# Kernel tuning notes

Hardware: AMD Instinct MI355X
Metric: run time of the kernel (lower is better)

The kernel has to match this reference:

```python
import jax, jax.numpy as jnp
import numpy as np

B, L, LTXT = 4, 1024, 128
D_MODEL, TEXT_DIM = 768, 768
D_INNER, D_STATE, D_CONV, DT_RANK = 2 * D_MODEL, 16, 4, (D_MODEL + 15) // 16


def setup_inputs() -> dict:
    key = jax.random.key(0)
    ks = jax.random.split(key, 10)
    s = 0.02
    f32 = jnp.float32
    # A_log init as in mamba_ssm: A = repeat(arange(1, d_state+1))
    A_log = jnp.log(jnp.broadcast_to(jnp.arange(1, D_STATE + 1, dtype=f32), (D_INNER, D_STATE)))
    return {
        "image_tokens": jax.random.normal(ks[0], (B, L, D_MODEL), f32),
        "text_tokens": jax.random.normal(ks[1], (B, LTXT, TEXT_DIM), f32),
        "W_txt": s * jax.random.normal(ks[2], (D_MODEL, TEXT_DIM), f32),
        "b_txt": jnp.zeros((D_MODEL,), f32),
        "in_proj_w": s * jax.random.normal(ks[3], (2 * D_INNER, D_MODEL), f32),
        "conv_w": s * jax.random.normal(ks[4], (D_INNER, 1, D_CONV), f32),
        "conv_b": jnp.zeros((D_INNER,), f32),
        "x_proj_w": s * jax.random.normal(ks[5], (DT_RANK + 2 * D_STATE, D_INNER), f32),
        "dt_proj_w": s * jax.random.normal(ks[6], (D_INNER, DT_RANK), f32),
        "dt_proj_b": jnp.full((D_INNER,), -4.6, f32),  # inv-softplus of small dt init
        "A_log": A_log,
        "D": jnp.ones((D_INNER,), f32),
        "out_proj_w": s * jax.random.normal(ks[7], (D_MODEL, D_INNER), f32),
    }


def _mamba(tokens, in_proj_w, conv_w, conv_b, x_proj_w, dt_proj_w, dt_proj_b, A_log, D, out_proj_w):
    Bsz = tokens.shape[0]
    # input projection -> x, z each (B, L, d_inner)
    xz = tokens @ in_proj_w.T
    x, z = jnp.split(xz, 2, axis=-1)
    # causal depthwise conv1d over L + SiLU
    x_bdl = jnp.transpose(x, (0, 2, 1))  # (B, d_inner, L)
    x_conv = jax.lax.conv_general_dilated(
        x_bdl, conv_w, (1,), [(D_CONV - 1, 0)],
        dimension_numbers=("NCH", "OIH", "NCH"), feature_group_count=D_INNER,
    ) + conv_b[None, :, None]
    x = jax.nn.silu(jnp.transpose(x_conv, (0, 2, 1)))  # (B, L, d_inner)
    # input-dependent SSM params
    x_dbl = x @ x_proj_w.T  # (B, L, dt_rank + 2*d_state)
    dt_r = x_dbl[..., :DT_RANK]
    Bm = x_dbl[..., DT_RANK:DT_RANK + D_STATE]  # (B, L, d_state)
    Cm = x_dbl[..., DT_RANK + D_STATE:]         # (B, L, d_state)
    dt = jax.nn.softplus(dt_r @ dt_proj_w.T + dt_proj_b)  # (B, L, d_inner)
    A = -jnp.exp(A_log)  # (d_inner, d_state)

    def step(h, inp):
        dt_t, B_t, C_t, u_t = inp  # (B,d_inner),(B,d_state),(B,d_state),(B,d_inner)
        dA = jnp.exp(dt_t[:, :, None] * A)                  # (B, d_inner, d_state)
        h = dA * h + (dt_t * u_t)[:, :, None] * B_t[:, None, :]
        y = jnp.einsum("bds,bs->bd", h, C_t)
        return h, y

    h0 = jnp.zeros((Bsz, D_INNER, D_STATE), tokens.dtype)
    xs = (
        jnp.transpose(dt, (1, 0, 2)),
        jnp.transpose(Bm, (1, 0, 2)),
        jnp.transpose(Cm, (1, 0, 2)),
        jnp.transpose(x, (1, 0, 2)),
    )
    _, ys = jax.lax.scan(step, h0, xs)  # ys: (L, B, d_inner)
    y = jnp.transpose(ys, (1, 0, 2)) + x * D
    y = y * jax.nn.silu(z)
    return y @ out_proj_w.T  # (B, L, d_model)


def reference(image_tokens, text_tokens, W_txt, b_txt, in_proj_w, conv_w, conv_b,
              x_proj_w, dt_proj_w, dt_proj_b, A_log, D, out_proj_w):
    # text_pool='cls' -> take token 0
    txt = text_tokens[:, 0, :] @ W_txt.T + b_txt          # (B, d_model)
    tokens = image_tokens + txt[:, None, :]                # broadcast add
    y = _mamba(tokens, in_proj_w, conv_w, conv_b, x_proj_w,
               dt_proj_w, dt_proj_b, A_log, D, out_proj_w)
    # AdaptiveAvgPool1d(1) over sequence dim, then squeeze -> (B, d_model)
    return y.mean(axis=1)
```

## Files before the change

kernel.cpp:

```cpp
#include <hip/hip_runtime.h>
#include <math.h>

constexpr int kB   = 4;
constexpr int kL   = 1024;
constexpr int kDM  = 768;
constexpr int kDI  = 1536;
constexpr int kDS  = 16;
constexpr int kDTR = 48;
constexpr int kNX  = 80;
constexpr int kM   = kB * kL;
constexpr int kLTXT = 128;

typedef __attribute__((ext_vector_type(8))) short bf16x8;
typedef __attribute__((ext_vector_type(4))) float f32x4;

__device__ inline unsigned short f2bf(float f) {
    unsigned u = __float_as_uint(f);
    u = (u + 0x7FFFu + ((u >> 16) & 1u)) >> 16;
    return (unsigned short)u;
}

__device__ __forceinline__ void gl2lds16(const unsigned short* g, unsigned short* l) {
    __builtin_amdgcn_global_load_lds(
        (const __attribute__((address_space(1))) unsigned int*)g,
        (__attribute__((address_space(3))) unsigned int*)l, 16, 0, 0);
}

__global__ __launch_bounds__(256) void txt_kernel(
    const float* __restrict__ text, const float* __restrict__ Wt,
    const float* __restrict__ bt, float* __restrict__ txt)
{
    int gw = blockIdx.x * 4 + (threadIdx.x >> 6);
    int lane = threadIdx.x & 63;
    int b = gw / kDM;
    int j = gw - b * kDM;
    const float* trow = text + (size_t)b * kLTXT * kDM;
    const float* wrow = Wt + (size_t)j * kDM;
    float acc = 0.f;
    for (int k = lane; k < kDM; k += 64) acc = fmaf(trow[k], wrow[k], acc);
    #pragma unroll
    for (int o = 32; o; o >>= 1) acc += __shfl_xor(acc, o, 64);
    if (lane == 0) txt[gw] = acc + bt[j];
}

__global__ __launch_bounds__(256) void tokens_bf16_kernel(
    const float* __restrict__ img, const float* __restrict__ txt,
    unsigned short* __restrict__ tok)
{
    int i = blockIdx.x * 256 + threadIdx.x;
    float4 a = ((const float4*)img)[i];
    int m = i / (kDM / 4);
    int k4 = i - m * (kDM / 4);
    float4 tv = ((const float4*)(txt + (size_t)(m >> 10) * kDM))[k4];
    ushort4 o;
    o.x = f2bf(a.x + tv.x); o.y = f2bf(a.y + tv.y);
    o.z = f2bf(a.z + tv.z); o.w = f2bf(a.w + tv.w);
    ((ushort4*)tok)[i] = o;
}

__global__ __launch_bounds__(256) void castw_kernel(
    const float* __restrict__ w, unsigned short* __restrict__ o, int n4)
{
    int i = blockIdx.x * 256 + threadIdx.x;
    if (i >= n4) return;
    float4 a = ((const float4*)w)[i];
    ushort4 v;
    v.x = f2bf(a.x); v.y = f2bf(a.y); v.z = f2bf(a.z); v.w = f2bf(a.w);
    ((ushort4*)o)[i] = v;
}

__global__ __launch_bounds__(256) void mfma_inproj_kernel(
    const unsigned short* __restrict__ A, const unsigned short* __restrict__ W,
    float* __restrict__ xout, float* __restrict__ gout)
{
    __shared__ unsigned short Asm[2][128][32];
    __shared__ unsigned short Wsm[2][128][32];
    const int t = threadIdx.x;
    const int lane = t & 63;
    const int wv = t >> 6;
    const int wr = wv >> 1, wc = wv & 1;
    const int m0 = blockIdx.x * 128;
    const int n0 = blockIdx.y * 128;

    const int srow = lane >> 2;
    const int scol = (lane & 3) * 8;
    const unsigned short* agp  = A + (size_t)(m0 + wv * 32 + srow) * kDM + scol;
    const unsigned short* agp2 = agp + 16 * kDM;
    const unsigned short* wgp  = W + (size_t)(n0 + wv * 32 + srow) * kDM + scol;
    const unsigned short* wgp2 = wgp + 16 * kDM;

    auto stage = [&](int buf, int k0) {
        gl2lds16(agp  + k0, &Asm[buf][wv * 32][0]);
        gl2lds16(agp2 + k0, &Asm[buf][wv * 32 + 16][0]);
        gl2lds16(wgp  + k0, &Wsm[buf][wv * 32][0]);
        gl2lds16(wgp2 + k0, &Wsm[buf][wv * 32 + 16][0]);
    };

    f32x4 acc[4][4] = {};
    const int fr = lane & 15;
    const int fk = (lane >> 4) * 8;

    stage(0, 0);
    __syncthreads();

    int buf = 0;
    for (int k0 = 0; k0 < kDM; k0 += 32) {
        if (k0 + 32 < kDM) stage(buf ^ 1, k0 + 32);
        bf16x8 af[4], wf[4];
        #pragma unroll
        for (int i = 0; i < 4; ++i)
            af[i] = *(const bf16x8*)&Asm[buf][wr * 64 + i * 16 + fr][fk];
        #pragma unroll
        for (int j = 0; j < 4; ++j)
            wf[j] = *(const bf16x8*)&Wsm[buf][wc * 64 + j * 16 + fr][fk];
        #pragma unroll
        for (int i = 0; i < 4; ++i)
            #pragma unroll
            for (int j = 0; j < 4; ++j)
                acc[i][j] = __builtin_amdgcn_mfma_f32_16x16x32_bf16(af[i], wf[j], acc[i][j], 0, 0, 0);
        __syncthreads();
        buf ^= 1;
    }

    const int erow = (lane >> 4) * 4;
    const int ecol = lane & 15;
    #pragma unroll
    for (int i = 0; i < 4; ++i) {
        #pragma unroll
        for (int j = 0; j < 4; ++j) {
            const int gn = n0 + wc * 64 + j * 16 + ecol;
            #pragma unroll
            for (int q = 0; q < 4; ++q) {
                const int gm = m0 + wr * 64 + i * 16 + erow + q;
                float v = acc[i][j][q];
                if (gn < kDI) {
                    xout[(size_t)gm * kDI + gn] = v;
                } else {
                    gout[(size_t)gm * kDI + (gn - kDI)] = v / (1.f + __expf(-v));
                }
            }
        }
    }
}

constexpr int kKS   = 8;
constexpr int kKSEG = kDI / kKS;

__global__ __launch_bounds__(256) void xproj_splitk_kernel(
    const float* __restrict__ A, const float* __restrict__ W,
    float* __restrict__ part)
{
    __shared__ float As[16][68];
    __shared__ float Ws[16][84];
    const int t = threadIdx.x;
    const int m0 = blockIdx.x * 64;
    const int kbase = blockIdx.y * kKSEG;
    const int lrow = t >> 2, lk4 = (t & 3) << 2;
    const int ci = (t & 15) << 2;
    const int cj = (t >> 4) * 5;
    float acc[4][5] = {};
    const float* aptr = A + (size_t)(m0 + lrow) * kDI + kbase + lk4;

    for (int k0 = 0; k0 < kKSEG; k0 += 16) {
        float4 av = *(const float4*)(aptr + k0);
        if (k0) __syncthreads();
        As[lk4+0][lrow] = av.x; As[lk4+1][lrow] = av.y;
        As[lk4+2][lrow] = av.z; As[lk4+3][lrow] = av.w;
        #pragma unroll
        for (int i = 0; i < 5; ++i) {
            int idx = t + 256 * i;
            int n = idx % 80;
            int k = idx / 80;
            Ws[k][n] = W[(size_t)n * kDI + kbase + k0 + k];
        }
        __syncthreads();
        #pragma unroll
        for (int k = 0; k < 16; ++k) {
            const float4 a4 = *(const float4*)&As[k][ci];
            const float aa[4] = {a4.x, a4.y, a4.z, a4.w};
            float ww[5];
            #pragma unroll
            for (int j = 0; j < 5; ++j) ww[j] = Ws[k][cj + j];
            #pragma unroll
            for (int i = 0; i < 4; ++i)
                #pragma unroll
                for (int j = 0; j < 5; ++j)
                    acc[i][j] = fmaf(aa[i], ww[j], acc[i][j]);
        }
    }

    float* pbase = part + ((size_t)blockIdx.y * kM) * kNX;
    #pragma unroll
    for (int i = 0; i < 4; ++i)
        #pragma unroll
        for (int j = 0; j < 5; ++j)
            pbase[(size_t)(m0 + ci + i) * kNX + cj + j] = acc[i][j];
}

__global__ __launch_bounds__(256) void xproj_reduce_kernel(
    const float* __restrict__ part, float* __restrict__ xdbl)
{
    int i = blockIdx.x * 256 + threadIdx.x;
    float s = 0.f;
    #pragma unroll
    for (int k = 0; k < kKS; ++k) s += part[(size_t)k * kM * kNX + i];
    xdbl[i] = s;
}

__global__ __launch_bounds__(256) void conv_silu_kernel(
    const float* __restrict__ xraw, const float* __restrict__ cw,
    const float* __restrict__ cb, float* __restrict__ xout)
{
    int i = blockIdx.x * 256 + threadIdx.x;
    int d4 = i % (kDI / 4);
    int ml = i / (kDI / 4);
    int l = ml & (kL - 1);
    const int d = d4 * 4;
    float4 acc = *(const float4*)&cb[d];
    const float* base = xraw + (size_t)ml * kDI + d - 3 * (size_t)kDI;
    float4 w0 = *(const float4*)&cw[(d + 0) * 4];
    float4 w1 = *(const float4*)&cw[(d + 1) * 4];
    float4 w2 = *(const float4*)&cw[(d + 2) * 4];
    float4 w3 = *(const float4*)&cw[(d + 3) * 4];
    const float wj[4][4] = {{w0.x, w1.x, w2.x, w3.x}, {w0.y, w1.y, w2.y, w3.y},
                            {w0.z, w1.z, w2.z, w3.z}, {w0.w, w1.w, w2.w, w3.w}};
    #pragma unroll
    for (int j = 0; j < 4; ++j) {
        if (l - 3 + j >= 0) {
            float4 xv = *(const float4*)(base + (size_t)j * kDI);
            acc.x = fmaf(xv.x, wj[j][0], acc.x);
            acc.y = fmaf(xv.y, wj[j][1], acc.y);
            acc.z = fmaf(xv.z, wj[j][2], acc.z);
            acc.w = fmaf(xv.w, wj[j][3], acc.w);
        }
    }
    acc.x /= (1.f + __expf(-acc.x));
    acc.y /= (1.f + __expf(-acc.y));
    acc.z /= (1.f + __expf(-acc.z));
    acc.w /= (1.f + __expf(-acc.w));
    *(float4*)&xout[(size_t)ml * kDI + d] = acc;
}

constexpr int kT  = 64;
constexpr int kNC = kL / kT;
constexpr int kXP = 84;

__global__ __launch_bounds__(256) void scan3_kernel(
    const float* __restrict__ x, const float* __restrict__ g,
    const float* __restrict__ xdbl, const float* __restrict__ Wd,
    const float* __restrict__ dt_bias,
    const float* __restrict__ A_log, const float* __restrict__ Dvec,
    float* __restrict__ ysum)
{
    __shared__ float xdS[2][kT][kXP];
    __shared__ float uS [2][kT][16];
    __shared__ float gS [2][kT][16];
    __shared__ float dtS[2][kT][17];
    const int t = threadIdx.x;
    const int b  = blockIdx.x / 96;
    const int d0 = (blockIdx.x % 96) * 16;

    const int sl = t >> 2, sc = (t & 3) << 2;
    const float* x_base  = x  + ((size_t)b << 10) * kDI + d0;
    const float* g_base  = g  + ((size_t)b << 10) * kDI + d0;
    const float* xd_base = xdbl + ((size_t)b << 10) * kNX;

    const int s = t & 15;
    const int c = t >> 4;
    const int d = d0 + c;
    const float Aval = -__expf(A_log[d * kDS + s]);

    const int cc = t & 15, ii = t >> 4;
    float4 wreg[12];
    {
        const float* wrow = Wd + (size_t)(d0 + cc) * kDTR;
        #pragma unroll
        for (int i = 0; i < 12; ++i) wreg[i] = *(const float4*)(wrow + i * 4);
    }
    const float bn = dt_bias[d0 + cc];

    float4 r_u, r_g, r_xd[5];
    auto load_chunk = [&](int l0) {
        r_u = *(const float4*)(x_base + (size_t)(l0 + sl) * kDI + sc);
        r_g = *(const float4*)(g_base + (size_t)(l0 + sl) * kDI + sc);
        #pragma unroll
        for (int j = 0; j < 5; ++j) {
            int idx = t + 256 * j;
            int row = idx / 20, col4 = idx % 20;
            r_xd[j] = *(const float4*)(xd_base + (size_t)(l0 + row) * kNX + col4 * 4);
        }
    };
    auto store_chunk = [&](int bf) {
        *(float4*)&uS[bf][sl][sc] = r_u;
        *(float4*)&gS[bf][sl][sc] = r_g;
        #pragma unroll
        for (int j = 0; j < 5; ++j) {
            int idx = t + 256 * j;
            int row = idx / 20, col4 = idx % 20;
            *(float4*)&xdS[bf][row][col4 * 4] = r_xd[j];
        }
    };
    auto compute_dt = [&](int bf) {
        #pragma unroll
        for (int q = 0; q < 4; ++q) {
            const int i = ii * 4 + q;
            float a = bn;
            #pragma unroll
            for (int k4 = 0; k4 < 12; ++k4) {
                const float4 xv = *(const float4*)&xdS[bf][i][k4 * 4];
                a = fmaf(xv.x, wreg[k4].x, a);
                a = fmaf(xv.y, wreg[k4].y, a);
                a = fmaf(xv.z, wreg[k4].z, a);
                a = fmaf(xv.w, wreg[k4].w, a);
            }
            a = (a > 20.f) ? a : log1pf(__expf(a));
            dtS[bf][i][cc] = a;
        }
    };

    load_chunk(0);
    store_chunk(0);
    __syncthreads();
    compute_dt(0);
    __syncthreads();

    float h = 0.f, acc = 0.f, ug = 0.f;
    for (int ck = 0; ck < kNC; ++ck) {
        const int bu = ck & 1;
        if (ck + 1 < kNC) load_chunk((ck + 1) * kT);
        #pragma unroll 4
        for (int i = 0; i < kT; ++i) {
            const float dtv = dtS[bu][i][c];
            const float uv  = uS [bu][i][c];
            const float gv  = gS [bu][i][c];
            const float Bv  = xdS[bu][i][kDTR + s];
            const float Cv  = xdS[bu][i][kDTR + 16 + s];
            const float dA  = __expf(dtv * Aval);
            h   = fmaf(dA, h, dtv * uv * Bv);
            acc = fmaf(h * Cv, gv, acc);
            ug  = fmaf(uv, gv, ug);
        }
        if (ck + 1 < kNC) {
            store_chunk(bu ^ 1);
            __syncthreads();
            compute_dt(bu ^ 1);
            __syncthreads();
        }
    }

    #pragma unroll
    for (int o = 1; o < 16; o <<= 1) acc += __shfl_xor(acc, o, 64);
    if (s == 0) ysum[(size_t)b * kDI + d] = acc + Dvec[d] * ug;
}

__global__ __launch_bounds__(256) void final_kernel(
    const float* __restrict__ ysum, const float* __restrict__ Wout,
    float* __restrict__ out)
{
    int gw = blockIdx.x * 4 + (threadIdx.x >> 6);
    int lane = threadIdx.x & 63;
    int b = gw / kDM;
    int j = gw - b * kDM;
    const float* yrow = ysum + (size_t)b * kDI;
    const float* wrow = Wout + (size_t)j * kDI;
    float acc = 0.f;
    for (int k = lane; k < kDI; k += 64) acc = fmaf(yrow[k], wrow[k], acc);
    #pragma unroll
    for (int o = 32; o; o >>= 1) acc += __shfl_xor(acc, o, 64);
    if (lane == 0) out[gw] = acc * (1.f / (float)kL);
}

extern "C" void kernel_launch(void* const* d_in, const int* in_sizes, int n_in,
                              void* d_out, int out_size, void* d_ws, size_t ws_size,
                              hipStream_t stream)
{
    const float* image_tokens = (const float*)d_in[0];
    const float* text_tokens  = (const float*)d_in[1];
    const float* W_txt        = (const float*)d_in[2];
    const float* b_txt        = (const float*)d_in[3];
    const float* in_proj_w    = (const float*)d_in[4];
    const float* conv_w       = (const float*)d_in[5];
    const float* conv_b       = (const float*)d_in[6];
    const float* x_proj_w     = (const float*)d_in[7];
    const float* dt_proj_w    = (const float*)d_in[8];
    const float* dt_proj_b    = (const float*)d_in[9];
    const float* A_log        = (const float*)d_in[10];
    const float* Dvec         = (const float*)d_in[11];
    const float* out_proj_w   = (const float*)d_in[12];
    float* out = (float*)d_out;

    char* p = (char*)d_ws;
    float* txt = (float*)p;                       p += 12288;
    unsigned short* tokb = (unsigned short*)p;    p += (size_t)kM * kDM * 2;
    unsigned short* wb   = (unsigned short*)p;    p += (size_t)2 * kDI * kDM * 2;
    float* xraw = (float*)p;                      p += (size_t)kM * kDI * 4;
    float* gbuf = (float*)p;                      p += (size_t)kM * kDI * 4;
    float* xbuf = (float*)p;                      p += (size_t)kM * kDI * 4;
    float* xdbl = (float*)p;                      p += (size_t)kM * kNX * 4;
    float* ysum = (float*)p;                      p += (size_t)kB * kDI * 4;
    float* part = (float*)tokb;

    txt_kernel<<<dim3(kB * kDM / 4), dim3(256), 0, stream>>>(text_tokens, W_txt, b_txt, txt);

    tokens_bf16_kernel<<<dim3(kM * kDM / 4 / 256), dim3(256), 0, stream>>>(image_tokens, txt, tokb);

    castw_kernel<<<dim3((2 * kDI * kDM / 4 + 255) / 256), dim3(256), 0, stream>>>(
        in_proj_w, wb, 2 * kDI * kDM / 4);

    mfma_inproj_kernel<<<dim3(kM / 128, 2 * kDI / 128), dim3(256), 0, stream>>>(
        tokb, wb, xraw, gbuf);

    conv_silu_kernel<<<dim3(kM * kDI / 4 / 256), dim3(256), 0, stream>>>(
        xraw, conv_w, conv_b, xbuf);

    xproj_splitk_kernel<<<dim3(kM / 64, kKS), dim3(256), 0, stream>>>(xbuf, x_proj_w, part);
    xproj_reduce_kernel<<<dim3(kM * kNX / 256), dim3(256), 0, stream>>>(part, xdbl);

    scan3_kernel<<<dim3(kB * 96), dim3(256), 0, stream>>>(
        xbuf, gbuf, xdbl, dt_proj_w, dt_proj_b, A_log, Dvec, ysum);

    final_kernel<<<dim3(kB * kDM / 4), dim3(256), 0, stream>>>(ysum, out_proj_w, out);
}
```

Baseline: 221.2 us.

## Split selective scan into sequence segments with a combine pass

The scan is split into 8 sequence segments per (batch, channel-group), so eight times as many blocks run in parallel with shorter serial chains. Each segment records its cumulative decay, its final local state, its local output sum, and a decay-weighted C·g sum. A new combine kernel chains these to add the contribution of each segment's incoming state. This adds extra multiplies per step, a second launch and scratch traffic reused from the xraw buffer.

```diff
diff --git a/kernel.cpp b/kernel.cpp
--- a/kernel.cpp
+++ b/kernel.cpp
@@ -241,24 +241,32 @@
     *(float4*)&xout[(size_t)ml * kDI + d] = acc;
 }
 
-constexpr int kT  = 64;
-constexpr int kNC = kL / kT;
-constexpr int kXP = 84;
-
-__global__ __launch_bounds__(256) void scan3_kernel(
+constexpr int kNSEG = 8;
+constexpr int kSEGL = kL / kNSEG;
+constexpr int kT    = 64;
+constexpr int kNCS  = kSEGL / kT;
+constexpr int kXP   = 84;
+constexpr int kP    = kB * kDI * 16;
+
+__global__ __launch_bounds__(256) void scan4_kernel(
     const float* __restrict__ x, const float* __restrict__ g,
     const float* __restrict__ xdbl, const float* __restrict__ Wd,
-    const float* __restrict__ dt_bias,
-    const float* __restrict__ A_log, const float* __restrict__ Dvec,
-    float* __restrict__ ysum)
+    const float* __restrict__ dt_bias, const float* __restrict__ A_log,
+    float* __restrict__ PA, float* __restrict__ QA,
+    float* __restrict__ accA, float* __restrict__ wcA,
+    float* __restrict__ ugA)
 {
     __shared__ float xdS[2][kT][kXP];
     __shared__ float uS [2][kT][16];
     __shared__ float gS [2][kT][16];
     __shared__ float dtS[2][kT][17];
     const int t = threadIdx.x;
-    const int b  = blockIdx.x / 96;
-    const int d0 = (blockIdx.x % 96) * 16;
+    const int blk = blockIdx.x;
+    const int seg = blk & (kNSEG - 1);
+    const int bd  = blk >> 3;
+    const int b   = bd / 96;
+    const int d0  = (bd % 96) * 16;
+    const int lb  = seg * kSEGL;
 
     const int sl = t >> 2, sc = (t & 3) << 2;
     const float* x_base  = x  + ((size_t)b << 10) * kDI + d0;
@@ -318,16 +326,16 @@
         }
     };
 
-    load_chunk(0);
+    load_chunk(lb);
     store_chunk(0);
     __syncthreads();
     compute_dt(0);
     __syncthreads();
 
-    float h = 0.f, acc = 0.f, ug = 0.f;
-    for (int ck = 0; ck < kNC; ++ck) {
+    float h = 0.f, cp = 1.f, acc = 0.f, wc = 0.f, ug = 0.f;
+    for (int ck = 0; ck < kNCS; ++ck) {
         const int bu = ck & 1;
-        if (ck + 1 < kNC) load_chunk((ck + 1) * kT);
+        if (ck + 1 < kNCS) load_chunk(lb + (ck + 1) * kT);
         #pragma unroll 4
         for (int i = 0; i < kT; ++i) {
             const float dtv = dtS[bu][i][c];
@@ -336,11 +344,14 @@
             const float Bv  = xdS[bu][i][kDTR + s];
             const float Cv  = xdS[bu][i][kDTR + 16 + s];
             const float dA  = __expf(dtv * Aval);
-            h   = fmaf(dA, h, dtv * uv * Bv);
-            acc = fmaf(h * Cv, gv, acc);
+            h  = fmaf(dA, h, dtv * uv * Bv);
+            cp = cp * dA;
+            const float cg = Cv * gv;
+            acc = fmaf(h, cg, acc);
+            wc  = fmaf(cp, cg, wc);
             ug  = fmaf(uv, gv, ug);
         }
-        if (ck + 1 < kNC) {
+        if (ck + 1 < kNCS) {
             store_chunk(bu ^ 1);
             __syncthreads();
             compute_dt(bu ^ 1);
@@ -348,9 +359,37 @@
         }
     }
 
-    #pragma unroll
-    for (int o = 1; o < 16; o <<= 1) acc += __shfl_xor(acc, o, 64);
-    if (s == 0) ysum[(size_t)b * kDI + d] = acc + Dvec[d] * ug;
+    const int p = (((b * kDI + d) << 4) | s);
+    const size_t o = (size_t)seg * kP + p;
+    PA[o] = cp; QA[o] = h; accA[o] = acc; wcA[o] = wc;
+    if (s == 0) ugA[(size_t)seg * (kB * kDI) + b * kDI + d] = ug;
+}
+
+__global__ __launch_bounds__(256) void scan_combine_kernel(
+    const float* __restrict__ PA, const float* __restrict__ QA,
+    const float* __restrict__ accA, const float* __restrict__ wcA,
+    const float* __restrict__ ugA, const float* __restrict__ Dvec,
+    float* __restrict__ ysum)
+{
+    const int p = blockIdx.x * 256 + threadIdx.x;
+    const int s = p & 15;
+    const int bd = p >> 4;
+    float h = 0.f, tot = 0.f;
+    #pragma unroll
+    for (int seg = 0; seg < kNSEG; ++seg) {
+        const size_t o = (size_t)seg * kP + p;
+        tot += accA[o] + h * wcA[o];
+        h = fmaf(PA[o], h, QA[o]);
+    }
+    #pragma unroll
+    for (int o2 = 1; o2 < 16; o2 <<= 1) tot += __shfl_xor(tot, o2, 64);
+    if (s == 0) {
+        float ug = 0.f;
+        #pragma unroll
+        for (int seg = 0; seg < kNSEG; ++seg)
+            ug += ugA[(size_t)seg * (kB * kDI) + bd];
+        ysum[bd] = tot + Dvec[bd % kDI] * ug;
+    }
 }
 
 __global__ __launch_bounds__(256) void final_kernel(
@@ -399,6 +438,11 @@
     float* xdbl = (float*)p;                      p += (size_t)kM * kNX * 4;
     float* ysum = (float*)p;                      p += (size_t)kB * kDI * 4;
     float* part = (float*)tokb;
+    float* PA   = xraw;
+    float* QA   = PA + (size_t)kNSEG * kP;
+    float* accA = QA + (size_t)kNSEG * kP;
+    float* wcA  = accA + (size_t)kNSEG * kP;
+    float* ugA  = wcA + (size_t)kNSEG * kP;
 
     txt_kernel<<<dim3(kB * kDM / 4), dim3(256), 0, stream>>>(text_tokens, W_txt, b_txt, txt);
 
@@ -416,8 +460,11 @@
     xproj_splitk_kernel<<<dim3(kM / 64, kKS), dim3(256), 0, stream>>>(xbuf, x_proj_w, part);
     xproj_reduce_kernel<<<dim3(kM * kNX / 256), dim3(256), 0, stream>>>(part, xdbl);
 
-    scan3_kernel<<<dim3(kB * 96), dim3(256), 0, stream>>>(
-        xbuf, gbuf, xdbl, dt_proj_w, dt_proj_b, A_log, Dvec, ysum);
+    scan4_kernel<<<dim3(kB * 96 * kNSEG), dim3(256), 0, stream>>>(
+        xbuf, gbuf, xdbl, dt_proj_w, dt_proj_b, A_log,
+        PA, QA, accA, wcA, ugA);
+    scan_combine_kernel<<<dim3(kP / 256), dim3(256), 0, stream>>>(
+        PA, QA, accA, wcA, ugA, Dvec, ysum);
 
     final_kernel<<<dim3(kB * kDM / 4), dim3(256), 0, stream>>>(ysum, out_proj_w, out);
 }
```

After: 207.2 us. 1.07x faster.
